# Kernel optimization log

Measured on AMD Instinct MI355X. Metric: run time of the kernel, lower is better.

Reference implementation:

```python
import math
import jax, jax.numpy as jnp
import numpy as np

N_HEADS = 8
EMB = 512
BATCH = 256
NKEYS = 2048
NEG_INF = -jnp.inf


def setup_inputs() -> dict:
    key = jax.random.key(0)
    kq, kk, kv, kw, km = jax.random.split(key, 5)
    query = jax.random.normal(kq, (BATCH, 1, EMB), dtype=jnp.float32)
    keys = jax.random.normal(kk, (BATCH, NKEYS, EMB), dtype=jnp.float32)
    value = jax.random.normal(kv, (BATCH, NKEYS, EMB), dtype=jnp.float32)
    W_o = jax.random.normal(kw, (EMB, EMB), dtype=jnp.float32) / math.sqrt(EMB)
    mask = jax.random.randint(km, (BATCH, 1, NKEYS), 0, 2) == 1  # bool [B,1,K]
    return {"query": query, "key": keys, "value": value, "W_o": W_o, "mask": mask}


def _make_heads(v):
    # [B, N, D] -> [H, B, N, D/H]
    b, n, d = v.shape
    return v.reshape(b, n, N_HEADS, d // N_HEADS).transpose(2, 0, 1, 3)


def reference(query, key, value, W_o, mask):
    qh = _make_heads(query)            # [H, B, 1, dh]
    kh = _make_heads(key)              # [H, B, K, dh]
    vh = _make_heads(value)            # [H, B, K, dh]
    dh = qh.shape[-1]
    # scaled dot-product scores: [H, B, 1, K]
    u = jnp.einsum("hbqd,hbkd->hbqk", qh, kh) / math.sqrt(dh)
    # boolean masking: mask [B,1,K] broadcasts over heads
    logits = jnp.where(mask[None], NEG_INF, u)
    a = jax.nn.softmax(logits, axis=-1)            # [H, B, 1, K]
    oh = jnp.einsum("hbqk,hbkd->hbqd", a, vh)      # [H, B, 1, dh]
    # unmake heads: [H,B,1,dh] -> [B,1,H*dh]
    b = oh.shape[1]
    merged = oh.transpose(1, 2, 0, 3).reshape(b, 1, N_HEADS * dh)
    out = merged @ W_o.T                           # Linear, no bias
    return out
```

## Files before the change

kernel.cpp:

```cpp
#include <hip/hip_runtime.h>


#define NB    256
#define NK    2048
#define EMBD  512
#define NH    8
#define DH    64
#define ACP   520

__device__ __forceinline__ void barrier_lgkm() {
    asm volatile("s_waitcnt lgkmcnt(0)" ::: "memory");
    __builtin_amdgcn_s_barrier();
}

__device__ __forceinline__ float4 ld4(const float* p) {
    return *reinterpret_cast<const float4*>(p);
}

__global__ __launch_bounds__(1024) void attn_kernel(
    const float* __restrict__ q,
    const float* __restrict__ kptr,
    const float* __restrict__ vptr,
    const int* __restrict__ mask,
    float* __restrict__ merged)
{
    const int b    = blockIdx.x;
    const int t    = threadIdx.x;
    const int w    = t >> 6;
    const int lane = t & 63;
    const int hq   = lane >> 3;
    const int sub  = lane & 7;

    __shared__ int   klist[NK];
    __shared__ int   wavecnt[16];
    __shared__ float redl[16][NH];
    __shared__ float accb[16 * ACP];

    const float* qb = q + (size_t)b * EMBD + lane * 8;
    const float4 qa = ld4(qb);
    const float4 qc = ld4(qb + 4);
    const float* kb = kptr + (size_t)b * NK * EMBD + lane * 8;
    const float* vb = vptr + (size_t)b * NK * EMBD + lane * 8;
    const int*   mrow = mask + (size_t)b * NK;

    const int kA = w * 128 + lane;
    const int kB = kA + 64;
    const int mA = mrow[kA];
    const int mB = mrow[kB];
    const unsigned long long balA = __ballot(mA == 0);
    const unsigned long long balB = __ballot(mB == 0);
    if (lane == 0) wavecnt[w] = __popcll(balA) + __popcll(balB);
    barrier_lgkm();

    int off = 0, nun = 0;
    #pragma unroll
    for (int i = 0; i < 16; ++i) {
        const int c = wavecnt[i];
        off += (i < w) ? c : 0;
        nun += c;
    }
    const unsigned long long below = (1ull << lane) - 1ull;
    if (!mA) klist[off + __popcll(balA & below)] = kA;
    if (!mB) klist[off + __popcll(balA) + __popcll(balB & below)] = kB;
    barrier_lgkm();

    float lsum = 0.f;
    float4 a0 = {0.f, 0.f, 0.f, 0.f};
    float4 a1 = {0.f, 0.f, 0.f, 0.f};
    {
        int key0 = (w < nun) ? klist[w] : -1;
        int key1 = (w + 16 < nun) ? klist[w + 16] : -1;
        float4 ka = {0,0,0,0}, kc = {0,0,0,0};
        float4 va = {0,0,0,0}, vc = {0,0,0,0};
        if (key0 >= 0) {
            const float* kk = kb + (size_t)key0 * EMBD;
            const float* vv = vb + (size_t)key0 * EMBD;
            ka = ld4(kk); kc = ld4(kk + 4);
            va = ld4(vv); vc = ld4(vv + 4);
        }
        for (int slot = w; slot < nun; slot += 16) {
            float4 nka = {0,0,0,0}, nkc = {0,0,0,0};
            float4 nva = {0,0,0,0}, nvc = {0,0,0,0};
            if (key1 >= 0) {
                const float* kk = kb + (size_t)key1 * EMBD;
                const float* vv = vb + (size_t)key1 * EMBD;
                nka = ld4(kk); nkc = ld4(kk + 4);
                nva = ld4(vv); nvc = ld4(vv + 4);
            }
            const int key2 = (slot + 32 < nun) ? klist[slot + 32] : -1;
            float sv = qa.x * ka.x + qa.y * ka.y + qa.z * ka.z + qa.w * ka.w
                     + qc.x * kc.x + qc.y * kc.y + qc.z * kc.z + qc.w * kc.w;
            sv += __shfl_xor(sv, 1, 8);
            sv += __shfl_xor(sv, 2, 8);
            sv += __shfl_xor(sv, 4, 8);
            const float p = __expf(sv * 0.125f);
            lsum += p;
            a0.x = fmaf(p, va.x, a0.x); a0.y = fmaf(p, va.y, a0.y);
            a0.z = fmaf(p, va.z, a0.z); a0.w = fmaf(p, va.w, a0.w);
            a1.x = fmaf(p, vc.x, a1.x); a1.y = fmaf(p, vc.y, a1.y);
            a1.z = fmaf(p, vc.z, a1.z); a1.w = fmaf(p, vc.w, a1.w);
            key0 = key1; ka = nka; kc = nkc; va = nva; vc = nvc; key1 = key2;
        }
    }
    if (sub == 0) redl[w][hq] = lsum;

    *reinterpret_cast<float4*>(&accb[w * ACP + lane * 8])     = a0;
    *reinterpret_cast<float4*>(&accb[w * ACP + lane * 8 + 4]) = a1;
    barrier_lgkm();

    if (t < EMBD) {
        const int h = t >> 6;
        float den = 0.f;
        #pragma unroll
        for (int ww = 0; ww < 16; ++ww) den += redl[ww][h];
        float s = 0.f;
        #pragma unroll
        for (int ww = 0; ww < 16; ++ww) s += accb[ww * ACP + t];
        merged[(size_t)b * EMBD + t] = s / den;
    }
}

__global__ __launch_bounds__(256) void proj_kernel_split(
    const float* __restrict__ merged,
    const float* __restrict__ Wo,
    float* __restrict__ out)
{
    const int bt = blockIdx.x >> 3;
    const int jt = blockIdx.x & 7;
    const int t  = threadIdx.x;
    __shared__ float4 mrow[8 * 128];
    #pragma unroll
    for (int k = 0; k < 4; ++k) {
        const int idx = k * 256 + t;
        mrow[idx] = reinterpret_cast<const float4*>(
            merged + (size_t)bt * 8 * EMBD)[idx];
    }
    __syncthreads();

    const int j    = jt * 64 + (t & 63);
    const int brel = t >> 6;
    const float4* wrow = reinterpret_cast<const float4*>(Wo + (size_t)j * EMBD);
    const float4* m0 = &mrow[brel * 128];
    const float4* m1 = &mrow[(brel + 4) * 128];
    float s0 = 0.f, s1 = 0.f;
    #pragma unroll 4
    for (int i = 0; i < 128; ++i) {
        const float4 wv = wrow[i];
        const float4 x0 = m0[i];
        const float4 x1 = m1[i];
        s0 += wv.x * x0.x + wv.y * x0.y + wv.z * x0.z + wv.w * x0.w;
        s1 += wv.x * x1.x + wv.y * x1.y + wv.z * x1.z + wv.w * x1.w;
    }
    out[(size_t)(bt * 8 + brel) * EMBD + j] = s0;
    out[(size_t)(bt * 8 + brel + 4) * EMBD + j] = s1;
}

__global__ __launch_bounds__(256) void proj_kernel_inplace(
    const float* __restrict__ merged,
    const float* __restrict__ Wo,
    float* __restrict__ out)
{
    const int b = blockIdx.x;
    const int t = threadIdx.x;
    __shared__ float mrow[EMBD];
    *reinterpret_cast<float2*>(&mrow[t * 2]) =
        *reinterpret_cast<const float2*>(&merged[(size_t)b * EMBD + t * 2]);
    __syncthreads();

    const float4* mv = reinterpret_cast<const float4*>(mrow);
    #pragma unroll
    for (int half = 0; half < 2; ++half) {
        const int j = t + half * 256;
        const float4* wrow = reinterpret_cast<const float4*>(Wo + (size_t)j * EMBD);
        float s = 0.f;
        #pragma unroll 4
        for (int i = 0; i < EMBD / 4; ++i) {
            const float4 wv = wrow[i];
            const float4 qv = mv[i];
            s += wv.x * qv.x + wv.y * qv.y + wv.z * qv.z + wv.w * qv.w;
        }
        out[(size_t)b * EMBD + j] = s;
    }
}

extern "C" void kernel_launch(void* const* d_in, const int* in_sizes, int n_in,
                              void* d_out, int out_size, void* d_ws, size_t ws_size,
                              hipStream_t stream) {
    const float* q    = (const float*)d_in[0];
    const float* kptr = (const float*)d_in[1];
    const float* vptr = (const float*)d_in[2];
    const float* Wo   = (const float*)d_in[3];
    const int*   mask = (const int*)d_in[4];
    float* out = (float*)d_out;

    float* merged = (ws_size >= (size_t)NB * EMBD * sizeof(float))
                        ? (float*)d_ws : out;

    attn_kernel<<<NB, 1024, 0, stream>>>(q, kptr, vptr, mask, merged);
    if (merged != out)
        proj_kernel_split<<<NB, 256, 0, stream>>>(merged, Wo, out);
    else
        proj_kernel_inplace<<<NB, 256, 0, stream>>>(merged, Wo, out);
}
```

Before: 212.9 us.

## Split attention keys into chunks across blocks and merge partials in projection

Splits each batch row's keys into 8 chunks handled by separate 256-thread blocks, writing unnormalized partial sums and denominators to workspace. A new merge kernel combines the chunk partials, normalizes, and applies the output projection. This aims to raise occupancy and balance memory-bound K/V streaming across CUs, at the cost of extra partial writes and a reduction pass. It falls back to the old path when workspace is too small.

```diff
diff --git a/kernel.cpp b/kernel.cpp
--- a/kernel.cpp
+++ b/kernel.cpp
@@ -6,7 +6,10 @@
 #define EMBD  512
 #define NH    8
 #define DH    64
-#define ACP   520
+#define CHUNKS 8
+#define CKEYS  256
+#define PREC   520
+#define ACP    520
 
 __device__ __forceinline__ void barrier_lgkm() {
     asm volatile("s_waitcnt lgkmcnt(0)" ::: "memory");
@@ -15,6 +18,159 @@
 
 __device__ __forceinline__ float4 ld4(const float* p) {
     return *reinterpret_cast<const float4*>(p);
+}
+
+__global__ __launch_bounds__(256) void attn_chunk_kernel(
+    const float* __restrict__ q,
+    const float* __restrict__ kptr,
+    const float* __restrict__ vptr,
+    const int* __restrict__ mask,
+    float* __restrict__ partials)
+{
+    const int bid  = blockIdx.x;
+    const int b    = bid >> 3;
+    const int c    = bid & 7;
+    const int t    = threadIdx.x;
+    const int w    = t >> 6;
+    const int lane = t & 63;
+    const int hq   = lane >> 3;
+    const int sub  = lane & 7;
+
+    __shared__ int   klist[CKEYS];
+    __shared__ int   wavecnt[4];
+    __shared__ float redl[4][NH];
+    __shared__ float accb[4 * ACP];
+
+    const float* qb = q + (size_t)b * EMBD + lane * 8;
+    const float4 qa = ld4(qb);
+    const float4 qc = ld4(qb + 4);
+    const float* kb = kptr + (size_t)b * NK * EMBD + lane * 8;
+    const float* vb = vptr + (size_t)b * NK * EMBD + lane * 8;
+    const int*   mrow = mask + (size_t)b * NK + c * CKEYS;
+
+    const int myk = w * 64 + lane;
+    const int mk  = mrow[myk];
+    const unsigned long long bal = __ballot(mk == 0);
+    if (lane == 0) wavecnt[w] = __popcll(bal);
+    __syncthreads();
+    int off = 0, nun = 0;
+    #pragma unroll
+    for (int i = 0; i < 4; ++i) {
+        const int cc = wavecnt[i];
+        off += (i < w) ? cc : 0;
+        nun += cc;
+    }
+    const unsigned long long below = (1ull << lane) - 1ull;
+    if (!mk) klist[off + __popcll(bal & below)] = c * CKEYS + myk;
+    __syncthreads();
+
+    float lsum = 0.f;
+    float4 a0 = {0.f, 0.f, 0.f, 0.f};
+    float4 a1 = {0.f, 0.f, 0.f, 0.f};
+    {
+        int key0 = (w < nun) ? klist[w] : -1;
+        int key1 = (w + 4 < nun) ? klist[w + 4] : -1;
+        float4 ka = {0,0,0,0}, kc = {0,0,0,0};
+        float4 va = {0,0,0,0}, vc = {0,0,0,0};
+        if (key0 >= 0) {
+            const float* kk = kb + (size_t)key0 * EMBD;
+            const float* vv = vb + (size_t)key0 * EMBD;
+            ka = ld4(kk); kc = ld4(kk + 4);
+            va = ld4(vv); vc = ld4(vv + 4);
+        }
+        for (int slot = w; slot < nun; slot += 4) {
+            float4 nka = {0,0,0,0}, nkc = {0,0,0,0};
+            float4 nva = {0,0,0,0}, nvc = {0,0,0,0};
+            if (key1 >= 0) {
+                const float* kk = kb + (size_t)key1 * EMBD;
+                const float* vv = vb + (size_t)key1 * EMBD;
+                nka = ld4(kk); nkc = ld4(kk + 4);
+                nva = ld4(vv); nvc = ld4(vv + 4);
+            }
+            const int key2 = (slot + 8 < nun) ? klist[slot + 8] : -1;
+            float sv = qa.x * ka.x + qa.y * ka.y + qa.z * ka.z + qa.w * ka.w
+                     + qc.x * kc.x + qc.y * kc.y + qc.z * kc.z + qc.w * kc.w;
+            sv += __shfl_xor(sv, 1, 8);
+            sv += __shfl_xor(sv, 2, 8);
+            sv += __shfl_xor(sv, 4, 8);
+            const float p = __expf(sv * 0.125f);
+            lsum += p;
+            a0.x = fmaf(p, va.x, a0.x); a0.y = fmaf(p, va.y, a0.y);
+            a0.z = fmaf(p, va.z, a0.z); a0.w = fmaf(p, va.w, a0.w);
+            a1.x = fmaf(p, vc.x, a1.x); a1.y = fmaf(p, vc.y, a1.y);
+            a1.z = fmaf(p, vc.z, a1.z); a1.w = fmaf(p, vc.w, a1.w);
+            key0 = key1; ka = nka; kc = nkc; va = nva; vc = nvc; key1 = key2;
+        }
+    }
+    if (sub == 0) redl[w][hq] = lsum;
+    *reinterpret_cast<float4*>(&accb[w * ACP + lane * 8])     = a0;
+    *reinterpret_cast<float4*>(&accb[w * ACP + lane * 8 + 4]) = a1;
+    __syncthreads();
+
+    float* rec = partials + (size_t)bid * PREC;
+    if (t < NH)
+        rec[t] = redl[0][t] + redl[1][t] + redl[2][t] + redl[3][t];
+    const float s0 = accb[t] + accb[ACP + t] + accb[2 * ACP + t] + accb[3 * ACP + t];
+    const int t2 = t + 256;
+    const float s1 = accb[t2] + accb[ACP + t2] + accb[2 * ACP + t2] + accb[3 * ACP + t2];
+    rec[8 + t]  = s0;
+    rec[8 + t2] = s1;
+}
+
+__global__ __launch_bounds__(256) void merge_proj_kernel(
+    const float* __restrict__ partials,
+    const float* __restrict__ Wo,
+    float* __restrict__ out)
+{
+    const int bt = blockIdx.x >> 3;
+    const int jt = blockIdx.x & 7;
+    const int t  = threadIdx.x;
+    __shared__ float mrow[8][EMBD];
+    __shared__ float sden[64];
+
+    if (t < 64) {
+        const int bb = t >> 3, h = t & 7;
+        const float* base = partials + (size_t)((bt * 8 + bb) * 8) * PREC;
+        float d = 0.f;
+        #pragma unroll
+        for (int cc = 0; cc < 8; ++cc) d += base[cc * PREC + h];
+        sden[t] = d;
+    }
+    #pragma unroll
+    for (int e = 0; e < 16; ++e) {
+        const int idx = e * 256 + t;
+        const int bb = idx >> 9, el = idx & 511;
+        const float* base = partials + (size_t)((bt * 8 + bb) * 8) * PREC + 8 + el;
+        float s = 0.f;
+        #pragma unroll
+        for (int cc = 0; cc < 8; ++cc) s += base[cc * PREC];
+        mrow[bb][el] = s;
+    }
+    __syncthreads();
+    #pragma unroll
+    for (int e = 0; e < 16; ++e) {
+        const int idx = e * 256 + t;
+        const int bb = idx >> 9, el = idx & 511;
+        mrow[bb][el] /= sden[bb * 8 + (el >> 6)];
+    }
+    __syncthreads();
+
+    const int j    = jt * 64 + (t & 63);
+    const int brel = t >> 6;
+    const float4* wrow = reinterpret_cast<const float4*>(Wo + (size_t)j * EMBD);
+    const float4* m0 = reinterpret_cast<const float4*>(&mrow[brel][0]);
+    const float4* m1 = reinterpret_cast<const float4*>(&mrow[brel + 4][0]);
+    float s0 = 0.f, s1 = 0.f;
+    #pragma unroll 4
+    for (int i = 0; i < 128; ++i) {
+        const float4 wv = wrow[i];
+        const float4 x0 = m0[i];
+        const float4 x1 = m1[i];
+        s0 += wv.x * x0.x + wv.y * x0.y + wv.z * x0.z + wv.w * x0.w;
+        s1 += wv.x * x1.x + wv.y * x1.y + wv.z * x1.z + wv.w * x1.w;
+    }
+    out[(size_t)(bt * 8 + brel) * EMBD + j] = s0;
+    out[(size_t)(bt * 8 + brel + 4) * EMBD + j] = s1;
 }
 
 __global__ __launch_bounds__(1024) void attn_kernel(
@@ -103,7 +259,6 @@
         }
     }
     if (sub == 0) redl[w][hq] = lsum;
-
     *reinterpret_cast<float4*>(&accb[w * ACP + lane * 8])     = a0;
     *reinterpret_cast<float4*>(&accb[w * ACP + lane * 8 + 4]) = a1;
     barrier_lgkm();
@@ -118,41 +273,6 @@
         for (int ww = 0; ww < 16; ++ww) s += accb[ww * ACP + t];
         merged[(size_t)b * EMBD + t] = s / den;
     }
-}
-
-__global__ __launch_bounds__(256) void proj_kernel_split(
-    const float* __restrict__ merged,
-    const float* __restrict__ Wo,
-    float* __restrict__ out)
-{
-    const int bt = blockIdx.x >> 3;
-    const int jt = blockIdx.x & 7;
-    const int t  = threadIdx.x;
-    __shared__ float4 mrow[8 * 128];
-    #pragma unroll
-    for (int k = 0; k < 4; ++k) {
-        const int idx = k * 256 + t;
-        mrow[idx] = reinterpret_cast<const float4*>(
-            merged + (size_t)bt * 8 * EMBD)[idx];
-    }
-    __syncthreads();
-
-    const int j    = jt * 64 + (t & 63);
-    const int brel = t >> 6;
-    const float4* wrow = reinterpret_cast<const float4*>(Wo + (size_t)j * EMBD);
-    const float4* m0 = &mrow[brel * 128];
-    const float4* m1 = &mrow[(brel + 4) * 128];
-    float s0 = 0.f, s1 = 0.f;
-    #pragma unroll 4
-    for (int i = 0; i < 128; ++i) {
-        const float4 wv = wrow[i];
-        const float4 x0 = m0[i];
-        const float4 x1 = m1[i];
-        s0 += wv.x * x0.x + wv.y * x0.y + wv.z * x0.z + wv.w * x0.w;
-        s1 += wv.x * x1.x + wv.y * x1.y + wv.z * x1.z + wv.w * x1.w;
-    }
-    out[(size_t)(bt * 8 + brel) * EMBD + j] = s0;
-    out[(size_t)(bt * 8 + brel + 4) * EMBD + j] = s1;
 }
 
 __global__ __launch_bounds__(256) void proj_kernel_inplace(
@@ -193,12 +313,13 @@
     const int*   mask = (const int*)d_in[4];
     float* out = (float*)d_out;
 
-    float* merged = (ws_size >= (size_t)NB * EMBD * sizeof(float))
-                        ? (float*)d_ws : out;
-
-    attn_kernel<<<NB, 1024, 0, stream>>>(q, kptr, vptr, mask, merged);
-    if (merged != out)
-        proj_kernel_split<<<NB, 256, 0, stream>>>(merged, Wo, out);
-    else
-        proj_kernel_inplace<<<NB, 256, 0, stream>>>(merged, Wo, out);
-}
+    const size_t need = (size_t)NB * CHUNKS * PREC * sizeof(float);
+    if (ws_size >= need) {
+        float* partials = (float*)d_ws;
+        attn_chunk_kernel<<<NB * CHUNKS, 256, 0, stream>>>(q, kptr, vptr, mask, partials);
+        merge_proj_kernel<<<NB, 256, 0, stream>>>(partials, Wo, out);
+    } else {
+        attn_kernel<<<NB, 1024, 0, stream>>>(q, kptr, vptr, mask, out);
+        proj_kernel_inplace<<<NB, 256, 0, stream>>>(out, Wo, out);
+    }
+}
```

Measured after the change: 228.9 us. 1.08x slower.
